# Kernel tuning notes

Hardware: AMD Instinct MI355X
Metric: run time of the kernel (lower is better)

The kernel has to match this reference:

```python
import jax, jax.numpy as jnp
import numpy as np

BATCH, SEQ, IN_DIM = 512, 512, 64
H1, H2, OUT = 100, 100, 1


def setup_inputs() -> dict:
    key = jax.random.key(0)
    ks = jax.random.split(key, 7)
    s = lambda fan_in: 1.0 / np.sqrt(fan_in)
    return {
        "x":   jax.random.normal(ks[0], (BATCH, SEQ, IN_DIM), dtype=jnp.float32),
        "W1x": jax.random.normal(ks[1], (IN_DIM, H1), dtype=jnp.float32) * s(IN_DIM),
        "W1h": jax.random.normal(ks[2], (H1, H1), dtype=jnp.float32) * s(H1),
        "b1":  jnp.zeros((H1,), dtype=jnp.float32),
        "W2x": jax.random.normal(ks[3], (H1, H2), dtype=jnp.float32) * s(H1),
        "W2h": jax.random.normal(ks[4], (H2, H2), dtype=jnp.float32) * s(H2),
        "b2":  jnp.zeros((H2,), dtype=jnp.float32),
        "Wo":  jax.random.normal(ks[5], (H2, OUT), dtype=jnp.float32) * s(H2),
        "bo":  jnp.zeros((OUT,), dtype=jnp.float32),
    }


def reference(x, W1x, W1h, b1, W2x, W2h, b2, Wo, bo):
    # Two stacked SimpleRNN layers (tanh), fused in a single scan over time.
    # Keras SimpleRNN: h_t = tanh(x_t @ Wx + h_{t-1} @ Wh + b)
    B = x.shape[0]
    h1_0 = jnp.zeros((B, W1h.shape[0]), dtype=x.dtype)
    h2_0 = jnp.zeros((B, W2h.shape[0]), dtype=x.dtype)

    def step(carry, x_t):
        h1, h2 = carry
        h1 = jnp.tanh(x_t @ W1x + h1 @ W1h + b1)   # [B, H1]
        h2 = jnp.tanh(h1 @ W2x + h2 @ W2h + b2)    # [B, H2]
        return (h1, h2), None

    xs = jnp.swapaxes(x, 0, 1)                      # [T, B, D]
    (h1_T, h2_T), _ = jax.lax.scan(step, (h1_0, h2_0), xs)
    out = h2_T @ Wo + bo                            # [B, 1]
    return out, h1_T, h2_T
```

## Files before the change

kernel.cpp:

```cpp
#include <hip/hip_runtime.h>
#include <math.h>

#define T      512
#define NBATCH 512
#define IN_DIM 64
#define H      100
#define KP     208
#define PBYTES 832

__device__ __forceinline__ float fast_tanh(float a) {
    float e = __expf(2.0f * a);
    return 1.0f - 2.0f / (e + 1.0f);
}

#define DPPMOV(x, ctrl) __int_as_float(__builtin_amdgcn_update_dpp( \
        0, __float_as_int(x), (ctrl), 0xF, 0xF, true))

__device__ __forceinline__ float wvalc(const float* __restrict__ WA,
                                       const float* __restrict__ WB,
                                       int kA, int R, int col) {
    if (col >= H) return 0.f;
    if (R < kA) return WA[R * H + col];
    int rr = R - kA;
    return (rr < H) ? WB[rr * H + col] : 0.f;
}

__device__ __forceinline__ float4 wload4c(const float* __restrict__ WA,
                                          const float* __restrict__ WB,
                                          int kA, int R0, int col) {
    return make_float4(wvalc(WA, WB, kA, R0 + 0, col),
                       wvalc(WA, WB, kA, R0 + 1, col),
                       wvalc(WA, WB, kA, R0 + 2, col),
                       wvalc(WA, WB, kA, R0 + 3, col));
}


#define K16(X) X(0) X(1) X(2) X(3) X(4) X(5) X(6) X(7) \
               X(8) X(9) X(10) X(11) X(12) X(13) X(14) X(15)

#define WDECL(k) float4 w0_##k={0,0,0,0}, w1_##k={0,0,0,0}, w2_##k={0,0,0,0}; \
                 float wt##k = 0.f;
#define WLOAD(k) { const int ck_ = j + ((k) ^ cl);                \
    w0_##k = wload4c(WA, WB, kA,        4*l, ck_);                \
    w1_##k = wload4c(WA, WB, kA,  64 + 4*l, ck_);                 \
    w2_##k = wload4c(WA, WB, kA, 128 + 4*l, ck_);                 \
    wt##k  = wvalc (WA, WB, kA, 192 + l,   ck_); }

#define ADECL(k) float a##k = 0.f;
#define FR0(k) { a##k = fmaf(v0_.x, w0_##k.x, a##k); a##k = fmaf(v0_.y, w0_##k.y, a##k); \
                 a##k = fmaf(v0_.z, w0_##k.z, a##k); a##k = fmaf(v0_.w, w0_##k.w, a##k); }
#define FR1(k) { a##k = fmaf(v1_.x, w1_##k.x, a##k); a##k = fmaf(v1_.y, w1_##k.y, a##k); \
                 a##k = fmaf(v1_.z, w1_##k.z, a##k); a##k = fmaf(v1_.w, w1_##k.w, a##k); }
#define FR2(k) { a##k = fmaf(v2_.x, w2_##k.x, a##k); a##k = fmaf(v2_.y, w2_##k.y, a##k); \
                 a##k = fmaf(v2_.z, w2_##k.z, a##k); a##k = fmaf(v2_.w, w2_##k.w, a##k); }
#define FT(k)  { a##k = fmaf(vt_, wt##k, a##k); }

#define DOTCORE(P, hv) {                                                  \
    const float4 v0_ = *(const float4*)(rb + (P));                        \
    const float4 v1_ = *(const float4*)(rb + (P) + 256);                  \
    const float4 v2_ = *(const float4*)(rb + (P) + 512);                  \
    const float  vt_ = *(const float*)(tb + (P));                         \
    K16(ADECL)                                                            \
    K16(FR0) K16(FR1) K16(FR2)                                            \
    if (hasTail) { K16(FT) }                                              \
    float u0_ = a0  + DPPMOV(a1,  0xB1);                                  \
    float u1_ = a2  + DPPMOV(a3,  0xB1);                                  \
    float u2_ = a4  + DPPMOV(a5,  0xB1);                                  \
    float u3_ = a6  + DPPMOV(a7,  0xB1);                                  \
    float u4_ = a8  + DPPMOV(a9,  0xB1);                                  \
    float u5_ = a10 + DPPMOV(a11, 0xB1);                                  \
    float u6_ = a12 + DPPMOV(a13, 0xB1);                                  \
    float u7_ = a14 + DPPMOV(a15, 0xB1);                                  \
    float r0_ = u0_ + DPPMOV(u1_, 0x4E);                                  \
    float r1_ = u2_ + DPPMOV(u3_, 0x4E);                                  \
    float r2_ = u4_ + DPPMOV(u5_, 0x4E);                                  \
    float r3_ = u6_ + DPPMOV(u7_, 0x4E);                                  \
    float z0_ = r0_ + DPPMOV(r1_, 0x128);                                 \
    float z1_ = r2_ + DPPMOV(r3_, 0x128);                                 \
    float zz_ = z0_ + DPPMOV(DPPMOV(z1_, 0x141), 0x1B);                   \
    hv = fast_tanh(zz_ + bj); }

__global__ __launch_bounds__(256, 2)
void drnn_kernel(const float* __restrict__ x,
                 const float* __restrict__ W1x, const float* __restrict__ W1h,
                 const float* __restrict__ b1,
                 const float* __restrict__ W2x, const float* __restrict__ W2h,
                 const float* __restrict__ b2,
                 const float* __restrict__ Wo,  const float* __restrict__ bo,
                 float* __restrict__ out)
{
    __shared__ __align__(16) float in1[2][KP];
    __shared__ __align__(16) float in2[2][KP];

    const int tid  = threadIdx.x;
    const int b    = blockIdx.x;
    const int wv   = tid >> 6;
    const int l    = tid & 15;
    const int unit = tid >> 4;
    const bool comp  = (unit < 14);
    const bool isL1  = (unit < 7);
    const bool isX14 = (unit == 14);
    const bool isX15 = (unit == 15);
    const bool hasTail = (wv >= 1);

    const float* __restrict__ xrow = x + (size_t)b * T * IN_DIM;

    for (int k = tid; k < 2 * KP; k += 256) {
        (&in1[0][0])[k] = 0.f;
        (&in2[0][0])[k] = 0.f;
    }
    if (tid < IN_DIM) in1[0][tid] = xrow[tid];

    const float* __restrict__ WA = isL1 ? W1x : W2x;
    const float* __restrict__ WB = isL1 ? W1h : W2h;
    const int kA = isL1 ? IN_DIM : H;
    const int ul = isL1 ? unit : unit - 7;
    const int j  = 16 * ((ul < 7) ? ul : 0);
    const int cl = (l & 3) | ((l >> 1) & 4) | ((l & 4) << 1);
    const int n  = j + cl;
    const bool stok = (n < H);
    const int nc = stok ? n : H - 1;
    const float bj = comp ? (isL1 ? b1 : b2)[nc] : 0.f;

    K16(WDECL)
    if (comp) { K16(WLOAD) }

    const char* lb = (const char*)(isL1 ? &in1[0][0] : &in2[0][0]);
    const char* rb = lb + 16 * l;
    const char* tb = lb + 768 + 4 * l;

    char* stA = (char*)&in1[0][64 + nc];
    char* stB = (char*)&in2[0][nc];
    char* stC = (char*)&in2[0][100 + nc];

    float4 xr = {0.f, 0.f, 0.f, 0.f};
    if (isX14) xr = *(const float4*)(xrow + 1 * IN_DIM + 4 * l);
    if (isX15) xr = *(const float4*)(xrow + 2 * IN_DIM + 4 * l);
    char* xw14 = (char*)&in1[1][4 * l];
    char* xw15 = (char*)&in1[0][4 * l];

    __syncthreads();

    #pragma unroll 1
    for (int i = 0; i < T; i += 2) {
        if (comp) {
            float hv; DOTCORE(0, hv)
            if (isL1) {
                if (stok) { *(float*)(stA + PBYTES) = hv;
                            *(float*)(stB + PBYTES) = hv; }
            } else if (stok && i > 0) {
                *(float*)(stC + PBYTES) = hv;
            }
        } else if (isX14) {
            *(float4*)xw14 = xr;
            if (i + 3 < T) xr = *(const float4*)(xrow + (size_t)(i + 3) * IN_DIM + 4 * l);
        }
        __syncthreads();
        if (comp) {
            float hv; DOTCORE(PBYTES, hv)
            if (isL1) {
                if (stok) { *(float*)stA = hv; *(float*)stB = hv; }
            } else if (stok) {
                *(float*)stC = hv;
            }
        } else if (isX15) {
            *(float4*)xw15 = xr;
            if (i + 4 < T) xr = *(const float4*)(xrow + (size_t)(i + 4) * IN_DIM + 4 * l);
        }
        __syncthreads();
    }

    if (comp && !isL1) {
        float hv; DOTCORE(0, hv)
        if (stok) *(float*)(stC + PBYTES) = hv;
    }
    __syncthreads();

    if (tid < H)
        out[NBATCH + (size_t)b * H + tid] = in1[0][64 + tid];
    if (tid < H)
        out[NBATCH + (size_t)NBATCH * H + (size_t)b * H + tid] = in2[1][100 + tid];

    if (tid < 64) {
        float v = in2[1][100 + tid] * Wo[tid];
        if (tid + 64 < H) v += in2[1][100 + 64 + tid] * Wo[tid + 64];
        #pragma unroll
        for (int off = 32; off >= 1; off >>= 1) v += __shfl_down(v, off);
        if (tid == 0) out[b] = v + bo[0];
    }
}

extern "C" void kernel_launch(void* const* d_in, const int* in_sizes, int n_in,
                              void* d_out, int out_size, void* d_ws, size_t ws_size,
                              hipStream_t stream) {
    const float* x   = (const float*)d_in[0];
    const float* W1x = (const float*)d_in[1];
    const float* W1h = (const float*)d_in[2];
    const float* b1  = (const float*)d_in[3];
    const float* W2x = (const float*)d_in[4];
    const float* W2h = (const float*)d_in[5];
    const float* b2  = (const float*)d_in[6];
    const float* Wo  = (const float*)d_in[7];
    const float* bo  = (const float*)d_in[8];
    float* out = (float*)d_out;

    drnn_kernel<<<NBATCH, 256, 0, stream>>>(x, W1x, W1h, b1, W2x, W2h, b2,
                                            Wo, bo, out);
}
```

Measured before the change: 621.1 us.

## Double threads per block, halve output columns per 16-lane unit

Doubles the block to 512 threads so each 16-lane unit computes 8 output columns instead of 16, halving per-thread FMA count and register-resident weights in the serial recurrence. The DPP reduction tree is shortened to match, and the input-row prefetch now uses one wave loading scalars instead of two units loading float4. Layer-1 outputs are written by different lane halves to the two destinations instead of one lane writing both. This trades more waves and barrier participants per block, plus lower per-CU block residency, for a shorter per-step critical path.

```diff
diff --git a/kernel.cpp b/kernel.cpp
--- a/kernel.cpp
+++ b/kernel.cpp
@@ -35,52 +35,48 @@
 }
 
 
-#define K16(X) X(0) X(1) X(2) X(3) X(4) X(5) X(6) X(7) \
-               X(8) X(9) X(10) X(11) X(12) X(13) X(14) X(15)
+#define K8(X) X(0) X(1) X(2) X(3) X(4) X(5) X(6) X(7)
 
 #define WDECL(k) float4 w0_##k={0,0,0,0}, w1_##k={0,0,0,0}, w2_##k={0,0,0,0}; \
                  float wt##k = 0.f;
-#define WLOAD(k) { const int ck_ = j + ((k) ^ cl);                \
-    w0_##k = wload4c(WA, WB, kA,        4*l, ck_);                \
-    w1_##k = wload4c(WA, WB, kA,  64 + 4*l, ck_);                 \
-    w2_##k = wload4c(WA, WB, kA, 128 + 4*l, ck_);                 \
+#define WLOAD(k) { const int ck_ = j + ((k) ^ c3l);            \
+    w0_##k = wload4c(WA, WB, kA,       4*l, ck_);              \
+    w1_##k = wload4c(WA, WB, kA,  64 + 4*l, ck_);              \
+    w2_##k = wload4c(WA, WB, kA, 128 + 4*l, ck_);              \
     wt##k  = wvalc (WA, WB, kA, 192 + l,   ck_); }
 
 #define ADECL(k) float a##k = 0.f;
-#define FR0(k) { a##k = fmaf(v0_.x, w0_##k.x, a##k); a##k = fmaf(v0_.y, w0_##k.y, a##k); \
-                 a##k = fmaf(v0_.z, w0_##k.z, a##k); a##k = fmaf(v0_.w, w0_##k.w, a##k); }
-#define FR1(k) { a##k = fmaf(v1_.x, w1_##k.x, a##k); a##k = fmaf(v1_.y, w1_##k.y, a##k); \
-                 a##k = fmaf(v1_.z, w1_##k.z, a##k); a##k = fmaf(v1_.w, w1_##k.w, a##k); }
-#define FR2(k) { a##k = fmaf(v2_.x, w2_##k.x, a##k); a##k = fmaf(v2_.y, w2_##k.y, a##k); \
-                 a##k = fmaf(v2_.z, w2_##k.z, a##k); a##k = fmaf(v2_.w, w2_##k.w, a##k); }
+#define FR0(k) { a##k = fmaf(va.x, w0_##k.x, a##k); a##k = fmaf(va.y, w0_##k.y, a##k); \
+                 a##k = fmaf(va.z, w0_##k.z, a##k); a##k = fmaf(va.w, w0_##k.w, a##k); }
+#define FR1(k) { a##k = fmaf(va.x, w1_##k.x, a##k); a##k = fmaf(va.y, w1_##k.y, a##k); \
+                 a##k = fmaf(va.z, w1_##k.z, a##k); a##k = fmaf(va.w, w1_##k.w, a##k); }
+#define FR2(k) { a##k = fmaf(va.x, w2_##k.x, a##k); a##k = fmaf(va.y, w2_##k.y, a##k); \
+                 a##k = fmaf(va.z, w2_##k.z, a##k); a##k = fmaf(va.w, w2_##k.w, a##k); }
 #define FT(k)  { a##k = fmaf(vt_, wt##k, a##k); }
 
-#define DOTCORE(P, hv) {                                                  \
-    const float4 v0_ = *(const float4*)(rb + (P));                        \
-    const float4 v1_ = *(const float4*)(rb + (P) + 256);                  \
-    const float4 v2_ = *(const float4*)(rb + (P) + 512);                  \
-    const float  vt_ = *(const float*)(tb + (P));                         \
-    K16(ADECL)                                                            \
-    K16(FR0) K16(FR1) K16(FR2)                                            \
-    if (hasTail) { K16(FT) }                                              \
-    float u0_ = a0  + DPPMOV(a1,  0xB1);                                  \
-    float u1_ = a2  + DPPMOV(a3,  0xB1);                                  \
-    float u2_ = a4  + DPPMOV(a5,  0xB1);                                  \
-    float u3_ = a6  + DPPMOV(a7,  0xB1);                                  \
-    float u4_ = a8  + DPPMOV(a9,  0xB1);                                  \
-    float u5_ = a10 + DPPMOV(a11, 0xB1);                                  \
-    float u6_ = a12 + DPPMOV(a13, 0xB1);                                  \
-    float u7_ = a14 + DPPMOV(a15, 0xB1);                                  \
-    float r0_ = u0_ + DPPMOV(u1_, 0x4E);                                  \
-    float r1_ = u2_ + DPPMOV(u3_, 0x4E);                                  \
-    float r2_ = u4_ + DPPMOV(u5_, 0x4E);                                  \
-    float r3_ = u6_ + DPPMOV(u7_, 0x4E);                                  \
-    float z0_ = r0_ + DPPMOV(r1_, 0x128);                                 \
-    float z1_ = r2_ + DPPMOV(r3_, 0x128);                                 \
-    float zz_ = z0_ + DPPMOV(DPPMOV(z1_, 0x141), 0x1B);                   \
-    hv = fast_tanh(zz_ + bj); }
+#define DOT(P, hv) {                                              \
+    K8(ADECL)                                                     \
+    float4 va = *(const float4*)(rb + (P));                       \
+    K8(FR0)                                                       \
+    va = *(const float4*)(rb + (P) + 256);                        \
+    K8(FR1)                                                       \
+    va = *(const float4*)(rb + (P) + 512);                        \
+    K8(FR2)                                                       \
+    if (!isL1) {                                                  \
+        const float vt_ = *(const float*)(tb + (P));              \
+        K8(FT)                                                    \
+    }                                                             \
+    float u0_ = a0 + DPPMOV(a1, 0xB1);                            \
+    float u1_ = a2 + DPPMOV(a3, 0xB1);                            \
+    float u2_ = a4 + DPPMOV(a5, 0xB1);                            \
+    float u3_ = a6 + DPPMOV(a7, 0xB1);                            \
+    float r0_ = u0_ + DPPMOV(u1_, 0x4E);                          \
+    float r1_ = u2_ + DPPMOV(u3_, 0x4E);                          \
+    float z_  = r0_ + DPPMOV(r1_, 0x128);                         \
+    z_ += DPPMOV(DPPMOV(z_, 0x141), 0x1B);                        \
+    hv = fast_tanh(z_ + bj); }
 
-__global__ __launch_bounds__(256, 2)
+__global__ __launch_bounds__(512, 4)
 void drnn_kernel(const float* __restrict__ x,
                  const float* __restrict__ W1x, const float* __restrict__ W1h,
                  const float* __restrict__ b1,
@@ -92,20 +88,18 @@
     __shared__ __align__(16) float in1[2][KP];
     __shared__ __align__(16) float in2[2][KP];
 
-    const int tid  = threadIdx.x;
-    const int b    = blockIdx.x;
-    const int wv   = tid >> 6;
-    const int l    = tid & 15;
-    const int unit = tid >> 4;
-    const bool comp  = (unit < 14);
-    const bool isL1  = (unit < 7);
-    const bool isX14 = (unit == 14);
-    const bool isX15 = (unit == 15);
-    const bool hasTail = (wv >= 1);
+    const int tid    = threadIdx.x;
+    const int b      = blockIdx.x;
+    const int l      = tid & 15;
+    const int unit   = tid >> 4;
+    const int lane64 = tid & 63;
+    const bool comp  = (unit < 26);
+    const bool isL1  = (unit < 13);
+    const bool isXW  = (tid >= 448);
 
     const float* __restrict__ xrow = x + (size_t)b * T * IN_DIM;
 
-    for (int k = tid; k < 2 * KP; k += 256) {
+    for (int k = tid; k < 2 * KP; k += 512) {
         (&in1[0][0])[k] = 0.f;
         (&in2[0][0])[k] = 0.f;
     }
@@ -113,66 +107,55 @@
 
     const float* __restrict__ WA = isL1 ? W1x : W2x;
     const float* __restrict__ WB = isL1 ? W1h : W2h;
-    const int kA = isL1 ? IN_DIM : H;
-    const int ul = isL1 ? unit : unit - 7;
-    const int j  = 16 * ((ul < 7) ? ul : 0);
-    const int cl = (l & 3) | ((l >> 1) & 4) | ((l & 4) << 1);
-    const int n  = j + cl;
-    const bool stok = (n < H);
-    const int nc = stok ? n : H - 1;
+    const int kA  = isL1 ? IN_DIM : H;
+    const int ul  = isL1 ? unit : unit - 13;
+    const int j   = 8 * ((ul >= 0 && ul < 13) ? ul : 0);
+    const int c3l = (l & 3) | ((l >> 1) & 4);
+    const int n   = j + c3l;
+    const int nc  = (n < H) ? n : H - 1;
     const float bj = comp ? (isL1 ? b1 : b2)[nc] : 0.f;
 
-    K16(WDECL)
-    if (comp) { K16(WLOAD) }
+    K8(WDECL)
+    if (comp) { K8(WLOAD) }
 
-    const char* lb = (const char*)(isL1 ? &in1[0][0] : &in2[0][0]);
-    const char* rb = lb + 16 * l;
-    const char* tb = lb + 768 + 4 * l;
+    const char* rb = (const char*)(isL1 ? &in1[0][0] : &in2[0][0]) + 16 * l;
+    const char* tb = (const char*)&in2[0][0] + 768 + 4 * l;
 
-    char* stA = (char*)&in1[0][64 + nc];
-    char* stB = (char*)&in2[0][nc];
-    char* stC = (char*)&in2[0][100 + nc];
+    char* stp; bool dow;
+    if (isL1) { stp = (char*)((l & 4) ? &in2[0][n] : &in1[0][64 + n]);
+                dow = comp && (n < H); }
+    else      { stp = (char*)&in2[0][100 + n];
+                dow = comp && (n < H) && !(l & 4); }
 
-    float4 xr = {0.f, 0.f, 0.f, 0.f};
-    if (isX14) xr = *(const float4*)(xrow + 1 * IN_DIM + 4 * l);
-    if (isX15) xr = *(const float4*)(xrow + 2 * IN_DIM + 4 * l);
-    char* xw14 = (char*)&in1[1][4 * l];
-    char* xw15 = (char*)&in1[0][4 * l];
+    char* xw = (char*)&in1[0][lane64];
+    float xr = 0.f;
+    if (isXW) xr = xrow[IN_DIM + lane64];
 
     __syncthreads();
 
     #pragma unroll 1
     for (int i = 0; i < T; i += 2) {
         if (comp) {
-            float hv; DOTCORE(0, hv)
-            if (isL1) {
-                if (stok) { *(float*)(stA + PBYTES) = hv;
-                            *(float*)(stB + PBYTES) = hv; }
-            } else if (stok && i > 0) {
-                *(float*)(stC + PBYTES) = hv;
-            }
-        } else if (isX14) {
-            *(float4*)xw14 = xr;
-            if (i + 3 < T) xr = *(const float4*)(xrow + (size_t)(i + 3) * IN_DIM + 4 * l);
+            float hv; DOT(0, hv)
+            if (dow && (isL1 || i > 0)) *(float*)(stp + PBYTES) = hv;
+        } else if (isXW) {
+            *(float*)(xw + PBYTES) = xr;
+            if (i + 2 < T) xr = xrow[(size_t)(i + 2) * IN_DIM + lane64];
         }
         __syncthreads();
         if (comp) {
-            float hv; DOTCORE(PBYTES, hv)
-            if (isL1) {
-                if (stok) { *(float*)stA = hv; *(float*)stB = hv; }
-            } else if (stok) {
-                *(float*)stC = hv;
-            }
-        } else if (isX15) {
-            *(float4*)xw15 = xr;
-            if (i + 4 < T) xr = *(const float4*)(xrow + (size_t)(i + 4) * IN_DIM + 4 * l);
+            float hv; DOT(PBYTES, hv)
+            if (dow) *(float*)stp = hv;
+        } else if (isXW) {
+            *(float*)xw = xr;
+            if (i + 3 < T) xr = xrow[(size_t)(i + 3) * IN_DIM + lane64];
         }
         __syncthreads();
     }
 
     if (comp && !isL1) {
-        float hv; DOTCORE(0, hv)
-        if (stok) *(float*)(stC + PBYTES) = hv;
+        float hv; DOT(0, hv)
+        if (dow) *(float*)(stp + PBYTES) = hv;
     }
     __syncthreads();
 
@@ -204,6 +187,6 @@
     const float* bo  = (const float*)d_in[8];
     float* out = (float*)d_out;
 
-    drnn_kernel<<<NBATCH, 256, 0, stream>>>(x, W1x, W1h, b1, W2x, W2h, b2,
+    drnn_kernel<<<NBATCH, 512, 0, stream>>>(x, W1x, W1h, b1, W2x, W2h, b2,
                                             Wo, bo, out);
 }
```

After: 704.6 us. 13.4% more time.
